# Kernel tuning notes

Hardware: AMD Instinct MI355X
Metric: run time of the kernel (lower is better)

Reference implementation:

```python
import math
import jax, jax.numpy as jnp
import numpy as np

B, N, NC = 2, 2048, 256
C_S, C_COND, C_Z, C_H, H, PQK, PV = 384, 256, 128, 16, 12, 4, 8
BQ, BK = 32, 128
NBLK = N // BQ
INF, EPS = 1e5, 1e-8
CONCAT = C_Z // 4 + C_H + PV * 4  # per-head output feature dim


def _ln(x, w=None, b=None, eps=1e-5):
    mu = jnp.mean(x, -1, keepdims=True)
    var = jnp.mean((x - mu) ** 2, -1, keepdims=True)
    y = (x - mu) * jax.lax.rsqrt(var + eps)
    if w is not None:
        y = y * w
    if b is not None:
        y = y + b
    return y


def _quat_to_rot(q):
    w, x, y, z = q[..., 0], q[..., 1], q[..., 2], q[..., 3]
    r = jnp.stack([
        1 - 2 * (y * y + z * z), 2 * (x * y - w * z), 2 * (x * z + w * y),
        2 * (x * y + w * z), 1 - 2 * (x * x + z * z), 2 * (y * z - w * x),
        2 * (x * z - w * y), 2 * (y * z + w * x), 1 - 2 * (x * x + y * y),
    ], axis=-1)
    return r.reshape(q.shape[:-1] + (3, 3))


def setup_inputs() -> dict:
    key = jax.random.key(0)
    ks = jax.random.split(key, 24)
    p = lambda k, shp: 0.02 * jax.random.normal(k, shp, dtype=jnp.float32)
    quat = jax.random.normal(ks[5], (B, N, 4), dtype=jnp.float32)
    quat = quat / jnp.linalg.norm(quat, axis=-1, keepdims=True)
    hc = H * C_H
    return {
        "s": jax.random.normal(ks[0], (B, N, C_S), dtype=jnp.float32),
        "cond": jax.random.normal(ks[1], (B, NC, C_COND), dtype=jnp.float32),
        "z": jax.random.normal(ks[2], (B, NBLK, BQ, BK, C_Z), dtype=jnp.float32),
        "trans": jax.random.normal(ks[3], (B, N, 3), dtype=jnp.float32),
        "rots": _quat_to_rot(quat),
        "s_mask": jnp.ones((B, N), dtype=jnp.float32),
        "cond_to_s_idx": jax.random.randint(ks[4], (B, N), 0, NC),
        "ln_cond_w": jnp.ones((C_COND,), dtype=jnp.float32),
        "lin_cond_W": p(ks[6], (C_S, C_COND)),
        "lin_cond_b": jnp.zeros((C_S,), dtype=jnp.float32),
        "lin_cond_nb_W": p(ks[7], (C_S, C_COND)),
        "ln_z_w": jnp.ones((C_Z,), dtype=jnp.float32),
        "ln_z_b": jnp.zeros((C_Z,), dtype=jnp.float32),
        "Wq": p(ks[8], (hc, C_S)),
        "Wk": p(ks[9], (hc, C_S)),
        "Wv": p(ks[10], (hc, C_S)),
        "Wqp": p(ks[11], (H * PQK * 3, C_S)),
        "Wkvp": p(ks[12], (H * (PQK + PV) * 3, C_S)),
        "Wb": p(ks[13], (H, C_Z)),
        "Wdz": p(ks[14], (C_Z // 4, C_Z)),
        "head_weights": jnp.full((H,), 0.541324854612918, dtype=jnp.float32),
        "Wout": p(ks[15], (C_S, H * CONCAT)),
    }


def _forward(s, cond, z, trans, rots, s_mask, cond_to_s_idx,
             ln_cond_w, lin_cond_W, lin_cond_b, lin_cond_nb_W, ln_z_w, ln_z_b,
             Wq, Wk, Wv, Wqp, Wkvp, Wb, Wdz, head_weights, Wout):
    # ---- GatherAdaLN ----
    s_n = _ln(s)
    c_n = _ln(cond, ln_cond_w)
    idx3 = jnp.broadcast_to(cond_to_s_idx[..., None], (B, N, C_S))
    gate = jnp.take_along_axis(c_n @ lin_cond_W.T + lin_cond_b, idx3, axis=1) * s_mask[..., None]
    bias = jnp.take_along_axis(c_n @ lin_cond_nb_W.T, idx3, axis=1) * s_mask[..., None]
    s2 = s_n * jax.nn.sigmoid(gate) + bias
    # ---- pair LN ----
    zn = _ln(z, ln_z_w, ln_z_b)
    # ---- block gather (to_queries / to_keys) ----
    pad = (BK - BQ) // 2
    base = jnp.arange(NBLK)[:, None] * BQ + jnp.arange(BK)[None, :] - pad  # [NBLK, BK]
    validk = (base >= 0) & (base < N)
    kidx = jnp.clip(base, 0, N - 1)

    def to_q(x):
        return x.reshape((B, NBLK, BQ) + x.shape[2:])

    def to_k(x):
        g = x[:, kidx]  # [B, NBLK, BK, ...]
        vm = validk.reshape((1, NBLK, BK) + (1,) * (g.ndim - 3)).astype(g.dtype)
        return g * vm

    q_in, k_in = to_q(s2), to_k(s2)
    q_t, q_R = to_q(trans), to_q(rots)
    k_t = to_k(trans)
    k_R = jnp.where(validk[None, :, :, None, None], rots[:, kidx], jnp.eye(3, dtype=rots.dtype))
    # ---- scalar q/k/v ----
    q = (q_in @ Wq.T).reshape(B, NBLK, BQ, H, C_H)
    k = (k_in @ Wk.T).reshape(B, NBLK, BK, H, C_H)
    v = (k_in @ Wv.T).reshape(B, NBLK, BK, H, C_H)
    # ---- point q/k/v in global frames ----
    qp = (q_in @ Wqp.T).reshape(B, NBLK, BQ, H * PQK, 3)
    q_pts = (jnp.einsum('bnqij,bnqpj->bnqpi', q_R, qp) + q_t[..., None, :]).reshape(B, NBLK, BQ, H, PQK, 3)
    kvp = (k_in @ Wkvp.T).reshape(B, NBLK, BK, H * (PQK + PV), 3)
    kv_pts = (jnp.einsum('bnkij,bnkpj->bnkpi', k_R, kvp) + k_t[..., None, :]).reshape(B, NBLK, BK, H, PQK + PV, 3)
    k_pts, v_pts = kv_pts[..., :PQK, :], kv_pts[..., PQK:, :]
    # ---- logits ----
    b_bias = zn @ Wb.T  # [B,NBLK,BQ,BK,H]
    a = jnp.einsum('bnqhc,bnkhc->bnqkh', q, k) * math.sqrt(1.0 / (3 * C_H)) + b_bias * math.sqrt(1.0 / 3)
    # point bias (cdist form)
    pt = -2.0 * jnp.einsum('bnqhpd,bnkhpd->bnqkh', q_pts, k_pts)
    pt = pt + jnp.sum(q_pts ** 2, axis=(-1, -2))[..., None, :]
    pt = pt + jnp.sum(k_pts ** 2, axis=(-1, -2))[..., None, :, :]
    hw = jax.nn.softplus(head_weights) * math.sqrt(1.0 / (3 * (PQK * 9.0 / 2)))
    pt = pt * hw * (-0.5)
    qm = to_q(s_mask[..., None])  # [B,NBLK,BQ,1]
    km = to_k(s_mask[..., None])  # [B,NBLK,BK,1]
    amask = INF * (qm * jnp.swapaxes(km, -1, -2) - 1.0)  # [B,NBLK,BQ,BK]
    a = a + pt + amask[..., None]
    a = jax.nn.softmax(jnp.swapaxes(a, -1, -2), axis=-1)  # [B,NBLK,BQ,H,BK]
    # ---- outputs ----
    o = jnp.einsum('bnqhk,bnkhc->bnqhc', a, v).reshape(B, NBLK, BQ, H * C_H)
    o_pt = jnp.einsum('bnqhk,bnkhvc->bnqhvc', a, v_pts)
    o_pt = jnp.einsum('bnqij,bnqhvi->bnqhvj', q_R, o_pt - q_t[..., None, None, :])  # R^T (p - t)
    o_pt_norm = jnp.sqrt(jnp.sum(o_pt ** 2, -1) + EPS).reshape(B, NBLK, BQ, H * PV)
    o_pt_flat = o_pt.reshape(B, NBLK, BQ, H * PV * 3)
    pair_z = zn @ Wdz.T  # [B,NBLK,BQ,BK,C_Z//4]
    o_pair = jnp.einsum('bnqhk,bnqkc->bnqhc', a, pair_z).reshape(B, NBLK, BQ, H * (C_Z // 4))
    feats = jnp.concatenate([o, o_pt_flat, o_pt_norm, o_pair], axis=-1)
    return (feats @ Wout.T).reshape(B, N, C_S)


def reference(s, cond, z, trans, rots, s_mask, cond_to_s_idx,
              ln_cond_w, lin_cond_W, lin_cond_b, lin_cond_nb_W, ln_z_w, ln_z_b,
              Wq, Wk, Wv, Wqp, Wkvp, Wb, Wdz, head_weights, Wout):
    return _forward(s, cond, z, trans, rots, s_mask, cond_to_s_idx,
                    ln_cond_w, lin_cond_W, lin_cond_b, lin_cond_nb_W, ln_z_w, ln_z_b,
                    Wq, Wk, Wv, Wqp, Wkvp, Wb, Wdz, head_weights, Wout)
```

## Files before the change

### kernel.cpp

```cpp
#include <hip/hip_runtime.h>
#include <math.h>

constexpr int Bv = 2, Nv = 2048, NCv = 256;
constexpr int CSv = 384, CCONDv = 256;
constexpr int CHv = 16, Hv = 12, PQKv = 4, PVv = 8;
constexpr int BQv = 32, BKv = 128, NBLKv = 64;
constexpr int HC = Hv * CHv;
constexpr int QPD = Hv * PQKv * 3;
constexpr int FEAT = 960;
constexpr int PROJW = 1152;
constexpr int NPAD = 2144;
constexpr float S1 = 0.14433756729740643f;
constexpr float S2 = 0.5773502691896258f;
constexpr float HWS = 0.13608276348795434f;

typedef __attribute__((ext_vector_type(8))) short bf16x8;
typedef __attribute__((ext_vector_type(4))) float f32x4;

__device__ __forceinline__ short f2bf(float f) {
    unsigned u = __float_as_uint(f);
    u += 0x7FFF + ((u >> 16) & 1);
    return (short)(u >> 16);
}
__device__ __forceinline__ float bf2f(short s) {
    return __uint_as_float(((unsigned)(unsigned short)s) << 16);
}
__device__ __forceinline__ unsigned pk2(short lo, short hi) {
    return ((unsigned)(unsigned short)lo) | (((unsigned)(unsigned short)hi) << 16);
}

union BF8 { short s[8]; bf16x8 v; uint4 u; };

__device__ __forceinline__ float blockReduceSum(float v, volatile float* red, int t, int nthr) {
    #pragma unroll
    for (int off = 32; off > 0; off >>= 1) v += __shfl_down(v, off, 64);
    int wid = t >> 6, lane = t & 63, nw = nthr >> 6;
    __syncthreads();
    if (lane == 0) red[wid] = v;
    __syncthreads();
    float r = 0.f;
    for (int w = 0; w < nw; ++w) r += red[w];
    return r;
}

__global__ __launch_bounds__(256) void k_head(const float* __restrict__ Wq,
                                              const float* __restrict__ Wk,
                                              const float* __restrict__ Wv,
                                              const float* __restrict__ Wqp,
                                              const float* __restrict__ Wkvp,
                                              const float* __restrict__ Wg,
                                              const float* __restrict__ Wnb,
                                              short* __restrict__ wsW,
                                              short* __restrict__ wsW2,
                                              const float* __restrict__ Wb,
                                              const float* __restrict__ Wdz,
                                              const float* __restrict__ lnzw,
                                              const float* __restrict__ lnzb,
                                              short* __restrict__ wp,
                                              float* __restrict__ SB,
                                              const float* __restrict__ cond,
                                              const float* __restrict__ lncw,
                                              short* __restrict__ cnbf) {
    __shared__ float red[4];
    int bid = blockIdx.x;
    int t = threadIdx.x;
    if (bid < 624) {
        int off = (bid * 256 + t) * 4;
        const float* src;
        int rel;
        if (off < 442368) {
            rel = off;
            if (rel < 73728) src = Wq;
            else if (rel < 147456) { src = Wk; rel -= 73728; }
            else if (rel < 221184) { src = Wv; rel -= 147456; }
            else if (rel < 276480) { src = Wqp; rel -= 221184; }
            else { src = Wkvp; rel -= 276480; }
            float4 v = *(const float4*)(src + rel);
            *(uint2*)(wsW + off) = make_uint2(pk2(f2bf(v.x), f2bf(v.y)), pk2(f2bf(v.z), f2bf(v.w)));
        } else {
            int o2 = off - 442368;
            rel = o2;
            if (rel < 98304) src = Wg; else { src = Wnb; rel -= 98304; }
            float4 v = *(const float4*)(src + rel);
            *(uint2*)(wsW2 + o2) = make_uint2(pk2(f2bf(v.x), f2bf(v.y)), pk2(f2bf(v.z), f2bf(v.w)));
        }
    } else if (bid == 624) {
        if (t < 176) {
            int c = t >> 2, q = t & 3;
            const float* wrow = (c < 12) ? (Wb + (size_t)c * 128) : (Wdz + (size_t)(c - 12) * 128);
            float sacc = 0.f, bacc = 0.f;
            for (int i = q * 32; i < q * 32 + 32; ++i) {
                float wf = wrow[i] * lnzw[i];
                short bs = f2bf(wf);
                wp[c * 128 + i] = bs;
                sacc += bf2f(bs);
                bacc += lnzb[i] * wrow[i];
            }
            sacc += __shfl_xor(sacc, 1, 64); sacc += __shfl_xor(sacc, 2, 64);
            bacc += __shfl_xor(bacc, 1, 64); bacc += __shfl_xor(bacc, 2, 64);
            if (q == 0) { SB[c] = sacc; SB[48 + c] = bacc; }
        }
        for (int i = t; i < 512; i += 256) wp[44 * 128 + i] = 0;
        if (t >= 176 && t < 180) { SB[t - 132] = 0.f; SB[48 + t - 132] = 0.f; }
    } else {
        int row = bid - 625;
        float c = cond[row * CCONDv + t];
        float mu = blockReduceSum(c, red, t, 256) * (1.f / CCONDv);
        float d = c - mu;
        float var = blockReduceSum(d * d, red, t, 256) * (1.f / CCONDv);
        cnbf[row * CCONDv + t] = f2bf(d * rsqrtf(var + 1e-5f) * lncw[t]);
    }
}

__global__ __launch_bounds__(256) void k_gemm_bt(const short* __restrict__ A,
                                                 const short* __restrict__ B,
                                                 float* __restrict__ C,
                                                 int K, int ldc) {
    __shared__ short As[128 * 40];
    __shared__ short Bs[128 * 40];
    int t = threadIdx.x;
    int m0 = blockIdx.x * 128, n0 = blockIdx.y * 128;
    int wv = t >> 6, lane = t & 63, lr = lane & 15, quad = lane >> 4;
    int mq = (wv & 1) * 64, nq = (wv >> 1) * 64;
    f32x4 acc[4][4];
    #pragma unroll
    for (int i = 0; i < 4; ++i)
        #pragma unroll
        for (int j = 0; j < 4; ++j) acc[i][j] = 0;

    int r0 = t >> 2, c8 = (t & 3) * 8;
    int r1 = (t + 256) >> 2, c81 = ((t + 256) & 3) * 8;

    for (int k0 = 0; k0 < K; k0 += 32) {
        uint4 a0 = *(const uint4*)(A + (size_t)(m0 + r0) * K + k0 + c8);
        uint4 a1 = *(const uint4*)(A + (size_t)(m0 + r1) * K + k0 + c81);
        uint4 b0 = *(const uint4*)(B + (size_t)(n0 + r0) * K + k0 + c8);
        uint4 b1 = *(const uint4*)(B + (size_t)(n0 + r1) * K + k0 + c81);
        *(uint4*)&As[r0 * 40 + c8] = a0;
        *(uint4*)&As[r1 * 40 + c81] = a1;
        *(uint4*)&Bs[r0 * 40 + c8] = b0;
        *(uint4*)&Bs[r1 * 40 + c81] = b1;
        __syncthreads();
        bf16x8 af[4], bf[4];
        #pragma unroll
        for (int i = 0; i < 4; ++i) {
            af[i] = *(const bf16x8*)&As[(mq + i * 16 + lr) * 40 + quad * 8];
            bf[i] = *(const bf16x8*)&Bs[(nq + i * 16 + lr) * 40 + quad * 8];
        }
        #pragma unroll
        for (int i = 0; i < 4; ++i)
            #pragma unroll
            for (int j = 0; j < 4; ++j)
                acc[i][j] = __builtin_amdgcn_mfma_f32_16x16x32_bf16(af[i], bf[j], acc[i][j], 0, 0, 0);
        __syncthreads();
    }
    #pragma unroll
    for (int i = 0; i < 4; ++i) {
        #pragma unroll
        for (int j = 0; j < 4; ++j) {
            int col = n0 + nq + j * 16 + lr;
            #pragma unroll
            for (int r = 0; r < 4; ++r) {
                int row = m0 + mq + i * 16 + quad * 4 + r;
                C[(size_t)row * ldc + col] = acc[i][j][r];
            }
        }
    }
}

__global__ __launch_bounds__(128) void k_s2(const float* __restrict__ s,
                                            const float* __restrict__ gb,
                                            const float* __restrict__ bg,
                                            const int* __restrict__ cidx,
                                            const float* __restrict__ smask,
                                            short* __restrict__ s2bf) {
    __shared__ float red[4];
    int row = blockIdx.x;
    int t = threadIdx.x;
    const float* sr = s + (size_t)row * CSv;
    float x0 = sr[t], x1 = sr[t + 128], x2 = sr[t + 256];
    float mu = blockReduceSum(x0 + x1 + x2, red, t, 128) * (1.f / CSv);
    float d0 = x0 - mu, d1 = x1 - mu, d2 = x2 - mu;
    float var = blockReduceSum(d0 * d0 + d1 * d1 + d2 * d2, red, t, 128) * (1.f / CSv);
    float rs = rsqrtf(var + 1e-5f);
    int b = row / Nv;
    int ci = cidx[row];
    float m = smask[row];
    const float* gbr = gb + (size_t)(b * NCv + ci) * 768;
    float dd[3] = {d0, d1, d2};
    #pragma unroll
    for (int j = 0; j < 3; ++j) {
        int cc = t + j * 128;
        float sn = dd[j] * rs;
        float g = (gbr[cc] + bg[cc]) * m, bi = gbr[384 + cc] * m;
        s2bf[(size_t)row * CSv + cc] = f2bf(sn * (1.f / (1.f + expf(-g))) + bi);
    }
}

__global__ __launch_bounds__(192) void k_post(const float* __restrict__ proj,
                                              const float* __restrict__ rots,
                                              const float* __restrict__ trans,
                                              float* __restrict__ qpts,
                                              float* __restrict__ kpts,
                                              float* __restrict__ vpts,
                                              float* __restrict__ qsq,
                                              float* __restrict__ ksq) {
    __shared__ float R[9], tr[3];
    int row = blockIdx.x;
    int t = threadIdx.x;
    if (t < 9) R[t] = rots[(size_t)row * 9 + t];
    if (t < 3) tr[t] = trans[(size_t)row * 3 + t];
    __syncthreads();
    const float* pr = proj + (size_t)row * PROJW + 576;
    float x = pr[t * 3 + 0], y = pr[t * 3 + 1], z = pr[t * 3 + 2];
    float ox = R[0] * x + R[1] * y + R[2] * z + tr[0];
    float oy = R[3] * x + R[4] * y + R[5] * z + tr[1];
    float oz = R[6] * x + R[7] * y + R[8] * z + tr[2];
    float sq = ox * ox + oy * oy + oz * oz;
    if (t < 48) {
        qpts[(size_t)row * QPD + t * 3 + 0] = ox;
        qpts[(size_t)row * QPD + t * 3 + 1] = oy;
        qpts[(size_t)row * QPD + t * 3 + 2] = oz;
        float s4 = sq + __shfl_xor(sq, 1, 64);
        s4 += __shfl_xor(s4, 2, 64);
        if ((t & 3) == 0) qsq[(size_t)row * Hv + (t >> 2)] = s4;
    } else {
        int p = t - 48;
        int h = p / 12, pp = p % 12;
        if (pp < PQKv) {
            kpts[(size_t)row * QPD + (h * PQKv + pp) * 3 + 0] = ox;
            kpts[(size_t)row * QPD + (h * PQKv + pp) * 3 + 1] = oy;
            kpts[(size_t)row * QPD + (h * PQKv + pp) * 3 + 2] = oz;
            float s4 = sq + __shfl_xor(sq, 1, 64);
            s4 += __shfl_xor(s4, 2, 64);
            if (pp == 0) ksq[(size_t)row * Hv + h] = s4;
        } else {
            int vi = h * PVv + pp - PQKv;
            vpts[(size_t)row * (Hv * PVv * 3) + vi * 3 + 0] = ox;
            vpts[(size_t)row * (Hv * PVv * 3) + vi * 3 + 1] = oy;
            vpts[(size_t)row * (Hv * PVv * 3) + vi * 3 + 2] = oz;
        }
    }
}

__global__ __launch_bounds__(256) void k_zg(const float* __restrict__ z,
                                            const short* __restrict__ wp,
                                            const float* __restrict__ SB,
                                            short* __restrict__ bbias2,
                                            short* __restrict__ pairzT,
                                            const short* __restrict__ cnbf,
                                            const short* __restrict__ wsW2,
                                            float* __restrict__ gb) {
    extern __shared__ char smem[];
    int t = threadIdx.x;
    int bid = blockIdx.x;
    if (bid >= 4096) {
        short* As = (short*)smem;
        short* Bs = As + 128 * 40;
        int g = bid - 4096;
        int m0 = (g & 3) * 128, n0 = (g >> 2) * 128;
        const int K = CCONDv, ldc = 768;
        int wv = t >> 6, lane = t & 63, lr = lane & 15, quad = lane >> 4;
        int mq = (wv & 1) * 64, nq = (wv >> 1) * 64;
        f32x4 acc[4][4];
        #pragma unroll
        for (int i = 0; i < 4; ++i)
            #pragma unroll
            for (int j = 0; j < 4; ++j) acc[i][j] = 0;
        int r0 = t >> 2, c8 = (t & 3) * 8;
        int r1 = (t + 256) >> 2, c81 = ((t + 256) & 3) * 8;
        for (int k0 = 0; k0 < K; k0 += 32) {
            uint4 a0 = *(const uint4*)(cnbf + (size_t)(m0 + r0) * K + k0 + c8);
            uint4 a1 = *(const uint4*)(cnbf + (size_t)(m0 + r1) * K + k0 + c81);
            uint4 b0 = *(const uint4*)(wsW2 + (size_t)(n0 + r0) * K + k0 + c8);
            uint4 b1 = *(const uint4*)(wsW2 + (size_t)(n0 + r1) * K + k0 + c81);
            *(uint4*)&As[r0 * 40 + c8] = a0;
            *(uint4*)&As[r1 * 40 + c81] = a1;
            *(uint4*)&Bs[r0 * 40 + c8] = b0;
            *(uint4*)&Bs[r1 * 40 + c81] = b1;
            __syncthreads();
            bf16x8 af[4], bf[4];
            #pragma unroll
            for (int i = 0; i < 4; ++i) {
                af[i] = *(const bf16x8*)&As[(mq + i * 16 + lr) * 40 + quad * 8];
                bf[i] = *(const bf16x8*)&Bs[(nq + i * 16 + lr) * 40 + quad * 8];
            }
            #pragma unroll
            for (int i = 0; i < 4; ++i)
                #pragma unroll
                for (int j = 0; j < 4; ++j)
                    acc[i][j] = __builtin_amdgcn_mfma_f32_16x16x32_bf16(af[i], bf[j], acc[i][j], 0, 0, 0);
            __syncthreads();
        }
        #pragma unroll
        for (int i = 0; i < 4; ++i)
            #pragma unroll
            for (int j = 0; j < 4; ++j) {
                int col = n0 + nq + j * 16 + lr;
                #pragma unroll
                for (int r = 0; r < 4; ++r) {
                    int row = m0 + mq + i * 16 + quad * 4 + r;
                    gb[(size_t)row * ldc + col] = acc[i][j][r];
                }
            }
        return;
    }
    short* zbuf = (short*)smem;
    short* wbuf = zbuf + 128 * 136;
    float* muL  = (float*)(wbuf + 48 * 136);
    float* rsL  = muL + 128;
    float* SL   = rsL + 128;
    float* BL   = SL + 48;

    int bblk = bid >> 5, qq = bid & 31;
    size_t row0 = (size_t)bid * 128;

    for (int idx = t; idx < 768; idx += 256) {
        int c = idx >> 4, k8 = idx & 15;
        uint4 v = *(const uint4*)(wp + c * 128 + k8 * 8);
        *(uint4*)&wbuf[c * 136 + k8 * 8] = v;
    }
    if (t < 96) {
        float v = SB[t];
        if (t < 48) SL[t] = v; else BL[t - 48] = v;
    }

    const float4* zsrc = (const float4*)(z + row0 * 128);
    #pragma unroll
    for (int it = 0; it < 16; ++it) {
        int f = it * 256 + t;
        int r = f >> 5, c4 = f & 31;
        float4 v = zsrc[f];
        short s0 = f2bf(v.x), s1 = f2bf(v.y), s2v = f2bf(v.z), s3 = f2bf(v.w);
        *(uint2*)&zbuf[r * 136 + c4 * 4] = make_uint2(pk2(s0, s1), pk2(s2v, s3));
        float sm = v.x + v.y + v.z + v.w;
        float sq = v.x * v.x + v.y * v.y + v.z * v.z + v.w * v.w;
        #pragma unroll
        for (int off = 1; off <= 16; off <<= 1) {
            sm += __shfl_xor(sm, off, 64);
            sq += __shfl_xor(sq, off, 64);
        }
        if ((t & 31) == 0) {
            float mu = sm * (1.f / 128.f);
            float var = sq * (1.f / 128.f) - mu * mu;
            muL[r] = mu;
            rsL[r] = rsqrtf(var + 1e-5f);
        }
    }
    __syncthreads();

    int wv = t >> 6, lane = t & 63;
    int lr = lane & 15, quad = lane >> 4;
    int mb = wv * 32;
    f32x4 acc[2][3];
    #pragma unroll
    for (int i = 0; i < 2; ++i)
        #pragma unroll
        for (int j = 0; j < 3; ++j) acc[i][j] = 0;
    #pragma unroll
    for (int kt = 0; kt < 4; ++kt) {
        int ko = kt * 32 + quad * 8;
        bf16x8 a0 = *(const bf16x8*)&zbuf[(mb + lr) * 136 + ko];
        bf16x8 a1 = *(const bf16x8*)&zbuf[(mb + 16 + lr) * 136 + ko];
        bf16x8 b0 = *(const bf16x8*)&wbuf[lr * 136 + ko];
        bf16x8 b1 = *(const bf16x8*)&wbuf[(16 + lr) * 136 + ko];
        bf16x8 b2 = *(const bf16x8*)&wbuf[(32 + lr) * 136 + ko];
        acc[0][0] = __builtin_amdgcn_mfma_f32_16x16x32_bf16(a0, b0, acc[0][0], 0, 0, 0);
        acc[0][1] = __builtin_amdgcn_mfma_f32_16x16x32_bf16(a0, b1, acc[0][1], 0, 0, 0);
        acc[0][2] = __builtin_amdgcn_mfma_f32_16x16x32_bf16(a0, b2, acc[0][2], 0, 0, 0);
        acc[1][0] = __builtin_amdgcn_mfma_f32_16x16x32_bf16(a1, b0, acc[1][0], 0, 0, 0);
        acc[1][1] = __builtin_amdgcn_mfma_f32_16x16x32_bf16(a1, b1, acc[1][1], 0, 0, 0);
        acc[1][2] = __builtin_amdgcn_mfma_f32_16x16x32_bf16(a1, b2, acc[1][2], 0, 0, 0);
    }

    short* bb_base = bbias2 + (size_t)(bblk * 12) * 4096 + qq * 128;
    short* pz_base = pairzT + (size_t)bid * 32 * 128;
    #pragma unroll
    for (int mt = 0; mt < 2; ++mt) {
        #pragma unroll
        for (int nt = 0; nt < 3; ++nt) {
            int col = nt * 16 + lr;
            int kbase = mb + mt * 16 + quad * 4;
            float ov[4];
            #pragma unroll
            for (int r4 = 0; r4 < 4; ++r4) {
                int rl = kbase + r4;
                ov[r4] = rsL[rl] * (acc[mt][nt][r4] - muL[rl] * SL[col]) + BL[col];
            }
            if (col < 12) {
                *(uint2*)&bb_base[(size_t)col * 4096 + kbase] =
                    make_uint2(pk2(f2bf(S2 * ov[0]), f2bf(S2 * ov[1])),
                               pk2(f2bf(S2 * ov[2]), f2bf(S2 * ov[3])));
            } else if (col < 44) {
                int c = col - 12;
                *(uint2*)&pz_base[c * 128 + kbase] =
                    make_uint2(pk2(f2bf(ov[0]), f2bf(ov[1])), pk2(f2bf(ov[2]), f2bf(ov[3])));
            }
        }
    }
}

__global__ __launch_bounds__(256) void k_kvcache(const float* __restrict__ proj,
                                                 const float* __restrict__ qpts,
                                                 const float* __restrict__ kpts,
                                                 const float* __restrict__ vpts,
                                                 const float* __restrict__ qsq,
                                                 const float* __restrict__ ksq,
                                                 const float* __restrict__ smask,
                                                 const float* __restrict__ head_w,
                                                 short* __restrict__ kc,
                                                 short* __restrict__ qc,
                                                 short* __restrict__ vTc,
                                                 float* __restrict__ cb,
                                                 float* __restrict__ rb,
                                                 float* __restrict__ kmp) {
    __shared__ short vt[40 * 136];
    int t = threadIdx.x;
    int tile = blockIdx.x % 17;
    int bh = blockIdx.x / 17;
    int b = bh / 12, h = bh % 12;
    float hw = log1pf(expf(head_w[h])) * HWS;
    int pn0 = tile * 128;
    int npn = (pn0 + 128 <= NPAD) ? 128 : (NPAD - pn0);

    for (int i = t; i < npn * 4; i += 256) {
        int r = i >> 2, q = i & 3;
        int pn = pn0 + r;
        int n = pn - 48; n = n < 0 ? 0 : (n > Nv - 1 ? Nv - 1 : n);
        size_t g = (size_t)b * Nv + n;
        BF8 o;
        if (q < 2) {
            const float* src = proj + g * PROJW + 192 + h * 16 + q * 8;
            #pragma unroll
            for (int j = 0; j < 8; ++j) o.s[j] = f2bf(src[j]);
        } else if (q == 2) {
            const float* src = kpts + g * QPD + h * 12;
            #pragma unroll
            for (int j = 0; j < 8; ++j) o.s[j] = f2bf(src[j]);
        } else {
            const float* src = kpts + g * QPD + h * 12 + 8;
            #pragma unroll
            for (int j = 0; j < 4; ++j) o.s[j] = f2bf(src[j]);
            o.s[4] = o.s[5] = o.s[6] = o.s[7] = 0;
        }
        *(uint4*)&kc[(((size_t)bh) * NPAD + pn) * 32 + q * 8] = o.u;
    }
    for (int i = t; i < npn; i += 256) {
        int pn = pn0 + i;
        int n = pn - 48; n = n < 0 ? 0 : (n > Nv - 1 ? Nv - 1 : n);
        size_t g = (size_t)b * Nv + n;
        cb[(size_t)bh * NPAD + pn] = -0.5f * hw * ksq[g * Hv + h];
        if (h == 0) kmp[(size_t)b * NPAD + pn] = (pn >= 48 && pn < 48 + Nv) ? smask[g] : 0.f;
    }
    for (int i = t; i < 512; i += 256) {
        int r = i >> 2, q = i & 3;
        int n = pn0 - 48 + r;
        if (n >= 0 && n < Nv) {
            size_t g = (size_t)b * Nv + n;
            BF8 o;
            if (q < 2) {
                const float* src = proj + g * PROJW + h * 16 + q * 8;
                #pragma unroll
                for (int j = 0; j < 8; ++j) o.s[j] = f2bf(S1 * src[j]);
            } else if (q == 2) {
                const float* src = qpts + g * QPD + h * 12;
                #pragma unroll
                for (int j = 0; j < 8; ++j) o.s[j] = f2bf(hw * src[j]);
            } else {
                const float* src = qpts + g * QPD + h * 12 + 8;
                #pragma unroll
                for (int j = 0; j < 4; ++j) o.s[j] = f2bf(hw * src[j]);
                o.s[4] = o.s[5] = o.s[6] = o.s[7] = 0;
            }
            *(uint4*)&qc[(((size_t)bh) * Nv + n) * 32 + q * 8] = o.u;
            if (q == 0) rb[(size_t)bh * Nv + n] = -0.5f * hw * qsq[g * Hv + h];
        }
    }
    for (int i = t; i < npn * 10; i += 256) {
        int r = i / 10, q = i % 10;
        int pn = pn0 + r;
        int n = pn - 48; n = n < 0 ? 0 : (n > Nv - 1 ? Nv - 1 : n);
        size_t g = (size_t)b * Nv + n;
        float4 v = (q < 4) ? *(const float4*)&proj[g * PROJW + 384 + h * 16 + q * 4]
                           : *(const float4*)&vpts[g * (Hv * PVv * 3) + h * 24 + (q - 4) * 4];
        int c0 = q * 4;
        vt[(c0 + 0) * 136 + r] = f2bf(v.x);
        vt[(c0 + 1) * 136 + r] = f2bf(v.y);
        vt[(c0 + 2) * 136 + r] = f2bf(v.z);
        vt[(c0 + 3) * 136 + r] = f2bf(v.w);
    }
    __syncthreads();
    for (int i = t; i < 640; i += 256) {
        int c = i >> 4, s = i & 15;
        if (s * 8 < npn)
            *(uint4*)&vTc[((size_t)bh * 40 + c) * NPAD + pn0 + s * 8] = *(const uint4*)&vt[c * 136 + s * 8];
    }
}

__global__ __launch_bounds__(512, 6) void k_attn_main(const short* __restrict__ kc,
                                                      const short* __restrict__ qc,
                                                      const short* __restrict__ vTc,
                                                      const float* __restrict__ cb,
                                                      const float* __restrict__ rb,
                                                      const float* __restrict__ kmp,
                                                      const float* __restrict__ smask,
                                                      const short* __restrict__ bbias2,
                                                      short* __restrict__ Aws,
                                                      float* __restrict__ optraw,
                                                      float* __restrict__ feats) {
    __shared__ short kfrag[128 * 40];
    __shared__ short qfrag[32 * 40];
    __shared__ short vtileT[48 * 136];
    __shared__ float sc[32 * 132];
    __shared__ short Abuf[32 * 136];
    __shared__ float rowb[32], qmL[32], colb[128], kmL[128];

    int t = threadIdx.x;
    int hp = blockIdx.x % 6;
    int bblk = blockIdx.x / 6;
    int b = bblk >> 6, blk = bblk & 63;
    int wv = t >> 6, lane = t & 63;
    int lr = lane & 15, quad = lane >> 4;
    int n0 = blk * BQv;

    if (t < 128) kmL[t] = kmp[(size_t)b * NPAD + n0 + t];
    if (t < 32)  qmL[t] = smask[(size_t)b * Nv + n0 + t];
    {
        int c = 40 + (t >> 6), k2 = (t & 63) * 2;
        *(unsigned*)&vtileT[c * 136 + k2] = 0;
    }
    __syncthreads();

    for (int hh = 0; hh < 2; ++hh) {
        int h = hp * 2 + hh;
        size_t bh = (size_t)b * 12 + h;

        {
            int r = t >> 2, s8 = (t & 3) * 8;
            *(uint4*)&kfrag[r * 40 + s8] = *(const uint4*)&kc[(bh * NPAD + n0 + r) * 32 + s8];
        }
        if (t < 128) {
            int r = t >> 2, s8 = (t & 3) * 8;
            *(uint4*)&qfrag[r * 40 + s8] = *(const uint4*)&qc[(bh * Nv + n0 + r) * 32 + s8];
        }
        if (t < 128) colb[t] = cb[bh * NPAD + n0 + t];
        if (t < 32)  rowb[t] = rb[bh * Nv + n0 + t];
        for (int i = t; i < 640; i += 512) {
            int c = i >> 4, s8 = (i & 15) * 8;
            *(uint4*)&vtileT[c * 136 + s8] = *(const uint4*)&vTc[(bh * 40 + c) * NPAD + n0 + s8];
        }
        __syncthreads();

        f32x4 d[2];
        d[0] = 0; d[1] = 0;
        {
            bf16x8 bfr = *(const bf16x8*)&kfrag[(wv * 16 + lr) * 40 + quad * 8];
            bf16x8 a0 = *(const bf16x8*)&qfrag[lr * 40 + quad * 8];
            bf16x8 a1 = *(const bf16x8*)&qfrag[(16 + lr) * 40 + quad * 8];
            d[0] = __builtin_amdgcn_mfma_f32_16x16x32_bf16(a0, bfr, d[0], 0, 0, 0);
            d[1] = __builtin_amdgcn_mfma_f32_16x16x32_bf16(a1, bfr, d[1], 0, 0, 0);
        }
        {
            const short* bb = bbias2 + (size_t)(bblk * 12 + h) * 4096;
            #pragma unroll
            for (int mt = 0; mt < 2; ++mt) {
                #pragma unroll
                for (int r = 0; r < 4; ++r) {
                    int q = mt * 16 + quad * 4 + r;
                    int k = wv * 16 + lr;
                    float logit = d[mt][r] + rowb[q] + colb[k]
                                + 1e5f * (qmL[q] * kmL[k] - 1.f)
                                + bf2f(bb[q * 128 + k]);
                    sc[q * 132 + k] = logit;
                }
            }
        }
        __syncthreads();

        {
            int q = t >> 4, i0 = (t & 15) * 8;
            float v[8];
            float m = -3.0e38f;
            #pragma unroll
            for (int j = 0; j < 8; ++j) { v[j] = sc[q * 132 + i0 + j]; m = fmaxf(m, v[j]); }
            #pragma unroll
            for (int off = 1; off <= 8; off <<= 1) m = fmaxf(m, __shfl_xor(m, off, 64));
            float ssum = 0.f;
            #pragma unroll
            for (int j = 0; j < 8; ++j) { v[j] = __expf(v[j] - m); ssum += v[j]; }
            #pragma unroll
            for (int off = 1; off <= 8; off <<= 1) ssum += __shfl_xor(ssum, off, 64);
            float inv = 1.f / ssum;
            short a8[8];
            #pragma unroll
            for (int j = 0; j < 8; ++j) a8[j] = f2bf(v[j] * inv);
            uint4 packed = make_uint4(pk2(a8[0], a8[1]), pk2(a8[2], a8[3]),
                                      pk2(a8[4], a8[5]), pk2(a8[6], a8[7]));
            *(uint4*)&Abuf[q * 136 + i0] = packed;
            *(uint4*)&Aws[((size_t)(bblk * 32 + q) * 12 + h) * 128 + i0] = packed;
        }
        __syncthreads();

        if (wv < 6) {
            int mt = wv & 1, nt = wv >> 1;
            f32x4 acc = 0;
            #pragma unroll
            for (int kt = 0; kt < 4; ++kt) {
                bf16x8 a = *(const bf16x8*)&Abuf[(mt * 16 + lr) * 136 + quad * 8 + kt * 32];
                bf16x8 bv = *(const bf16x8*)&vtileT[(nt * 16 + lr) * 136 + quad * 8 + kt * 32];
                acc = __builtin_amdgcn_mfma_f32_16x16x32_bf16(a, bv, acc, 0, 0, 0);
            }
            int c = nt * 16 + lr;
            #pragma unroll
            for (int r = 0; r < 4; ++r) {
                int q = mt * 16 + quad * 4 + r;
                size_t nqg = (size_t)b * Nv + n0 + q;
                if (c < 16) feats[nqg * FEAT + h * 16 + c] = acc[r];
                else if (c < 40) optraw[nqg * 288 + h * 24 + (c - 16)] = acc[r];
            }
        }
        __syncthreads();
    }
}

__global__ __launch_bounds__(64) void k_pair(const short* __restrict__ Aws,
                                             const short* __restrict__ pairzT,
                                             const float* __restrict__ optraw,
                                             const float* __restrict__ rots,
                                             const float* __restrict__ trans,
                                             float* __restrict__ feats) {
    __shared__ float Rt[12];
    int t = threadIdx.x;
    int bid = blockIdx.x;
    int lr = t & 15, quad = t >> 4;

    if (t < 9) Rt[t] = rots[(size_t)bid * 9 + t];
    if (t < 3) Rt[9 + t] = trans[(size_t)bid * 3 + t];
    __syncthreads();

    const short* Ab = Aws + (size_t)bid * 1536;
    const short* Pb = pairzT + (size_t)bid * 4096;
    f32x4 acc0 = 0, acc1 = 0;
    #pragma unroll
    for (int kt = 0; kt < 4; ++kt) {
        int ko = kt * 32 + quad * 8;
        bf16x8 a = 0;
        if (lr < 12) a = *(const bf16x8*)&Ab[lr * 128 + ko];
        bf16x8 b0 = *(const bf16x8*)&Pb[lr * 128 + ko];
        bf16x8 b1 = *(const bf16x8*)&Pb[(16 + lr) * 128 + ko];
        acc0 = __builtin_amdgcn_mfma_f32_16x16x32_bf16(a, b0, acc0, 0, 0, 0);
        acc1 = __builtin_amdgcn_mfma_f32_16x16x32_bf16(a, b1, acc1, 0, 0, 0);
    }
    float* frow = feats + (size_t)bid * FEAT;
    #pragma unroll
    for (int r = 0; r < 4; ++r) {
        int hh = quad * 4 + r;
        if (hh < 12) {
            frow[576 + hh * 32 + lr] = acc0[r];
            frow[576 + hh * 32 + 16 + lr] = acc1[r];
        }
    }

    for (int p = t; p < 96; p += 64) {
        float x = optraw[(size_t)bid * 288 + p * 3 + 0] - Rt[9];
        float y = optraw[(size_t)bid * 288 + p * 3 + 1] - Rt[10];
        float z = optraw[(size_t)bid * 288 + p * 3 + 2] - Rt[11];
        float lx = Rt[0] * x + Rt[3] * y + Rt[6] * z;
        float ly = Rt[1] * x + Rt[4] * y + Rt[7] * z;
        float lz = Rt[2] * x + Rt[5] * y + Rt[8] * z;
        frow[192 + p * 3 + 0] = lx;
        frow[192 + p * 3 + 1] = ly;
        frow[192 + p * 3 + 2] = lz;
        frow[480 + p] = sqrtf(lx * lx + ly * ly + lz * lz + 1e-8f);
    }
}

__global__ __launch_bounds__(256) void k_out(const float* __restrict__ A,
                                             const float* __restrict__ Wo,
                                             float* __restrict__ C) {
    __shared__ float As[32][68];
    __shared__ float Bs[32][68];
    int t = threadIdx.x;
    int m0 = blockIdx.x * 64;
    int c0 = blockIdx.y * 64;
    int tx = t & 15, ty = t >> 4;
    int lr = t >> 2, lk = (t & 3) * 8;
    float acc[4][4] = {};
    for (int k0 = 0; k0 < FEAT; k0 += 32) {
        const float4* ap = (const float4*)(A + (size_t)(m0 + lr) * FEAT + k0 + lk);
        const float4* bp = (const float4*)(Wo + (size_t)(c0 + lr) * FEAT + k0 + lk);
        float4 a0 = ap[0], a1 = ap[1];
        float4 b0 = bp[0], b1 = bp[1];
        As[lk + 0][lr] = a0.x; As[lk + 1][lr] = a0.y; As[lk + 2][lr] = a0.z; As[lk + 3][lr] = a0.w;
        As[lk + 4][lr] = a1.x; As[lk + 5][lr] = a1.y; As[lk + 6][lr] = a1.z; As[lk + 7][lr] = a1.w;
        Bs[lk + 0][lr] = b0.x; Bs[lk + 1][lr] = b0.y; Bs[lk + 2][lr] = b0.z; Bs[lk + 3][lr] = b0.w;
        Bs[lk + 4][lr] = b1.x; Bs[lk + 5][lr] = b1.y; Bs[lk + 6][lr] = b1.z; Bs[lk + 7][lr] = b1.w;
        __syncthreads();
        #pragma unroll
        for (int kk = 0; kk < 32; ++kk) {
            float4 a4 = *(const float4*)&As[kk][ty * 4];
            float4 b4 = *(const float4*)&Bs[kk][tx * 4];
            float av[4] = {a4.x, a4.y, a4.z, a4.w};
            float bv[4] = {b4.x, b4.y, b4.z, b4.w};
            #pragma unroll
            for (int i = 0; i < 4; ++i)
                #pragma unroll
                for (int j = 0; j < 4; ++j) acc[i][j] += av[i] * bv[j];
        }
        __syncthreads();
    }
    #pragma unroll
    for (int i = 0; i < 4; ++i)
        #pragma unroll
        for (int j = 0; j < 4; ++j)
            C[(size_t)(m0 + ty * 4 + i) * CSv + c0 + tx * 4 + j] = acc[i][j];
}

extern "C" void kernel_launch(void* const* d_in, const int* in_sizes, int n_in,
                              void* d_out, int out_size, void* d_ws, size_t ws_size,
                              hipStream_t stream) {
    const float* s          = (const float*)d_in[0];
    const float* cond       = (const float*)d_in[1];
    const float* z          = (const float*)d_in[2];
    const float* trans      = (const float*)d_in[3];
    const float* rots       = (const float*)d_in[4];
    const float* smask      = (const float*)d_in[5];
    const int*   cidx       = (const int*)d_in[6];
    const float* ln_cond_w  = (const float*)d_in[7];
    const float* lin_cond_W = (const float*)d_in[8];
    const float* lin_cond_b = (const float*)d_in[9];
    const float* lin_cond_nb_W = (const float*)d_in[10];
    const float* ln_z_w     = (const float*)d_in[11];
    const float* ln_z_b     = (const float*)d_in[12];
    const float* Wq         = (const float*)d_in[13];
    const float* Wk         = (const float*)d_in[14];
    const float* Wv         = (const float*)d_in[15];
    const float* Wqp        = (const float*)d_in[16];
    const float* Wkvp       = (const float*)d_in[17];
    const float* Wb         = (const float*)d_in[18];
    const float* Wdz        = (const float*)d_in[19];
    const float* head_w     = (const float*)d_in[20];
    const float* Wout       = (const float*)d_in[21];
    float* out = (float*)d_out;

    float* p = (float*)d_ws;
    short* wp = (short*)p; p += 3072;
    float* SBp = p; p += 96;
    short* wsW  = (short*)p; p += 221184;
    short* wsW2 = (short*)p; p += 98304;
    short* cnbf = (short*)p; p += 65536;
    float* gb   = p; p += (size_t)512 * 768;
    short* s2bf = (short*)p; p += (size_t)Bv * Nv * CSv / 2;
    float* proj = p; p += (size_t)Bv * Nv * PROJW;
    float* qpts = p; p += (size_t)Bv * Nv * QPD;
    float* kpts = p; p += (size_t)Bv * Nv * QPD;
    float* vpts = p; p += (size_t)Bv * Nv * (Hv * PVv * 3);
    float* qsq  = p; p += (size_t)Bv * Nv * Hv;
    float* ksq  = p; p += (size_t)Bv * Nv * Hv;
    short* bbias2 = (short*)p; p += (size_t)128 * 12 * 4096 / 2;
    short* pairzT = (short*)p; p += (size_t)128 * 32 * 32 * 64;
    short* Aws    = (short*)p; p += (size_t)4096 * 12 * 64;
    float* optraw = p; p += (size_t)4096 * 288;
    float* feats  = p; p += (size_t)Bv * Nv * FEAT;
    short* kc  = (short*)p; p += (size_t)Bv * 12 * NPAD * 32 / 2;
    short* qc  = (short*)p; p += (size_t)Bv * 12 * Nv * 32 / 2;
    short* vTc = (short*)p; p += (size_t)Bv * 12 * 40 * NPAD / 2;
    float* cbw = p; p += (size_t)Bv * 12 * NPAD;
    float* rbw = p; p += (size_t)Bv * 12 * Nv;
    float* kmp = p; p += (size_t)Bv * NPAD;

    k_head<<<1137, 256, 0, stream>>>(Wq, Wk, Wv, Wqp, Wkvp, lin_cond_W, lin_cond_nb_W,
                                     wsW, wsW2, Wb, Wdz, ln_z_w, ln_z_b, wp, SBp,
                                     cond, ln_cond_w, cnbf);
    k_zg<<<4120, 256, 49280, stream>>>(z, wp, SBp, bbias2, pairzT, cnbf, wsW2, gb);
    k_s2<<<Bv * Nv, 128, 0, stream>>>(s, gb, lin_cond_b, cidx, smask, s2bf);
    k_gemm_bt<<<dim3(32, 9), 256, 0, stream>>>(s2bf, wsW, proj, CSv, PROJW);
    k_post<<<Bv * Nv, 192, 0, stream>>>(proj, rots, trans, qpts, kpts, vpts, qsq, ksq);
    k_kvcache<<<Bv * 12 * 17, 256, 0, stream>>>(proj, qpts, kpts, vpts, qsq, ksq,
                                                smask, head_w, kc, qc, vTc, cbw, rbw, kmp);
    k_attn_main<<<Bv * NBLKv * 6, 512, 0, stream>>>(kc, qc, vTc, cbw, rbw, kmp, smask,
                                                    bbias2, Aws, optraw, feats);
    k_pair<<<Bv * NBLKv * BQv, 64, 0, stream>>>(Aws, pairzT, optraw, rots, trans, feats);
    k_out<<<dim3(64, 6), 256, 0, stream>>>(feats, Wout, out);
}
```

Baseline: 580.3 us.

## Move output projection to split-bf16 MFMA and halve projection GEMM N-tile

Replaces the FP32 SIMT output GEMM with an MFMA kernel that splits both operands into bf16 hi/lo parts and sums three products, keeping close to FP32 accuracy. Wout is pre-split once in the head kernel, using extra blocks. The projection GEMM switches to 128x64 tiles, doubling the block count to fill more CUs. The cost is three times the MFMA work, extra workspace, and per-tile conversion of the activations.

```diff
diff --git a/kernel.cpp b/kernel.cpp
--- a/kernel.cpp
+++ b/kernel.cpp
@@ -27,6 +27,10 @@
 }
 __device__ __forceinline__ unsigned pk2(short lo, short hi) {
     return ((unsigned)(unsigned short)lo) | (((unsigned)(unsigned short)hi) << 16);
+}
+__device__ __forceinline__ void split2(float x, short& hi, short& lo) {
+    hi = f2bf(x);
+    lo = f2bf(x - bf2f(hi));
 }
 
 union BF8 { short s[8]; bf16x8 v; uint4 u; };
@@ -60,7 +64,10 @@
                                               float* __restrict__ SB,
                                               const float* __restrict__ cond,
                                               const float* __restrict__ lncw,
-                                              short* __restrict__ cnbf) {
+                                              short* __restrict__ cnbf,
+                                              const float* __restrict__ Wout,
+                                              short* __restrict__ WoutH,
+                                              short* __restrict__ WoutL) {
     __shared__ float red[4];
     int bid = blockIdx.x;
     int t = threadIdx.x;
@@ -102,62 +109,65 @@
         }
         for (int i = t; i < 512; i += 256) wp[44 * 128 + i] = 0;
         if (t >= 176 && t < 180) { SB[t - 132] = 0.f; SB[48 + t - 132] = 0.f; }
-    } else {
+    } else if (bid < 1137) {
         int row = bid - 625;
         float c = cond[row * CCONDv + t];
         float mu = blockReduceSum(c, red, t, 256) * (1.f / CCONDv);
         float d = c - mu;
         float var = blockReduceSum(d * d, red, t, 256) * (1.f / CCONDv);
         cnbf[row * CCONDv + t] = f2bf(d * rsqrtf(var + 1e-5f) * lncw[t]);
-    }
-}
-
-__global__ __launch_bounds__(256) void k_gemm_bt(const short* __restrict__ A,
-                                                 const short* __restrict__ B,
-                                                 float* __restrict__ C,
-                                                 int K, int ldc) {
+    } else {
+        int off = ((bid - 1137) * 256 + t) * 4;
+        float4 v = *(const float4*)(Wout + off);
+        short h0, l0, h1, l1, h2, l2, h3, l3;
+        split2(v.x, h0, l0); split2(v.y, h1, l1); split2(v.z, h2, l2); split2(v.w, h3, l3);
+        *(uint2*)(WoutH + off) = make_uint2(pk2(h0, h1), pk2(h2, h3));
+        *(uint2*)(WoutL + off) = make_uint2(pk2(l0, l1), pk2(l2, l3));
+    }
+}
+
+__global__ __launch_bounds__(256) void k_gemm_proj(const short* __restrict__ A,
+                                                   const short* __restrict__ B,
+                                                   float* __restrict__ C) {
     __shared__ short As[128 * 40];
-    __shared__ short Bs[128 * 40];
+    __shared__ short Bs[64 * 40];
+    const int K = CSv, ldc = PROJW;
     int t = threadIdx.x;
-    int m0 = blockIdx.x * 128, n0 = blockIdx.y * 128;
+    int m0 = blockIdx.x * 128, n0 = blockIdx.y * 64;
     int wv = t >> 6, lane = t & 63, lr = lane & 15, quad = lane >> 4;
-    int mq = (wv & 1) * 64, nq = (wv >> 1) * 64;
-    f32x4 acc[4][4];
+    int mq = (wv & 1) * 64, nq = (wv >> 1) * 32;
+    f32x4 acc[4][2];
     #pragma unroll
     for (int i = 0; i < 4; ++i)
         #pragma unroll
-        for (int j = 0; j < 4; ++j) acc[i][j] = 0;
+        for (int j = 0; j < 2; ++j) acc[i][j] = 0;
 
     int r0 = t >> 2, c8 = (t & 3) * 8;
-    int r1 = (t + 256) >> 2, c81 = ((t + 256) & 3) * 8;
 
     for (int k0 = 0; k0 < K; k0 += 32) {
         uint4 a0 = *(const uint4*)(A + (size_t)(m0 + r0) * K + k0 + c8);
-        uint4 a1 = *(const uint4*)(A + (size_t)(m0 + r1) * K + k0 + c81);
+        uint4 a1 = *(const uint4*)(A + (size_t)(m0 + r0 + 64) * K + k0 + c8);
         uint4 b0 = *(const uint4*)(B + (size_t)(n0 + r0) * K + k0 + c8);
-        uint4 b1 = *(const uint4*)(B + (size_t)(n0 + r1) * K + k0 + c81);
         *(uint4*)&As[r0 * 40 + c8] = a0;
-        *(uint4*)&As[r1 * 40 + c81] = a1;
+        *(uint4*)&As[(r0 + 64) * 40 + c8] = a1;
         *(uint4*)&Bs[r0 * 40 + c8] = b0;
-        *(uint4*)&Bs[r1 * 40 + c81] = b1;
         __syncthreads();
-        bf16x8 af[4], bf[4];
-        #pragma unroll
-        for (int i = 0; i < 4; ++i) {
-            af[i] = *(const bf16x8*)&As[(mq + i * 16 + lr) * 40 + quad * 8];
-            bf[i] = *(const bf16x8*)&Bs[(nq + i * 16 + lr) * 40 + quad * 8];
-        }
+        bf16x8 af[4], bf[2];
+        #pragma unroll
+        for (int i = 0; i < 4; ++i) af[i] = *(const bf16x8*)&As[(mq + i * 16 + lr) * 40 + quad * 8];
+        #pragma unroll
+        for (int j = 0; j < 2; ++j) bf[j] = *(const bf16x8*)&Bs[(nq + j * 16 + lr) * 40 + quad * 8];
         #pragma unroll
         for (int i = 0; i < 4; ++i)
             #pragma unroll
-            for (int j = 0; j < 4; ++j)
+            for (int j = 0; j < 2; ++j)
                 acc[i][j] = __builtin_amdgcn_mfma_f32_16x16x32_bf16(af[i], bf[j], acc[i][j], 0, 0, 0);
         __syncthreads();
     }
     #pragma unroll
     for (int i = 0; i < 4; ++i) {
         #pragma unroll
-        for (int j = 0; j < 4; ++j) {
+        for (int j = 0; j < 2; ++j) {
             int col = n0 + nq + j * 16 + lr;
             #pragma unroll
             for (int r = 0; r < 4; ++r) {
@@ -675,45 +685,72 @@
     }
 }
 
-__global__ __launch_bounds__(256) void k_out(const float* __restrict__ A,
-                                             const float* __restrict__ Wo,
-                                             float* __restrict__ C) {
-    __shared__ float As[32][68];
-    __shared__ float Bs[32][68];
+__global__ __launch_bounds__(256) void k_out_mfma(const float* __restrict__ A,
+                                                  const short* __restrict__ BhG,
+                                                  const short* __restrict__ BlG,
+                                                  float* __restrict__ C) {
+    __shared__ short Ah[32 * 40];
+    __shared__ short Al[32 * 40];
+    __shared__ short Bh[128 * 40];
+    __shared__ short Bl[128 * 40];
     int t = threadIdx.x;
-    int m0 = blockIdx.x * 64;
-    int c0 = blockIdx.y * 64;
-    int tx = t & 15, ty = t >> 4;
-    int lr = t >> 2, lk = (t & 3) * 8;
-    float acc[4][4] = {};
+    int m0 = blockIdx.x * 32, c0 = blockIdx.y * 128;
+    int wv = t >> 6, lane = t & 63, lr = lane & 15, quad = lane >> 4;
+    int nq = wv * 32;
+    f32x4 acc[2][2];
+    acc[0][0] = 0; acc[0][1] = 0; acc[1][0] = 0; acc[1][1] = 0;
+
+    int ra = t >> 3, ca = (t & 7) * 4;
+    int rb = t >> 2, s8 = (t & 3) * 8;
+
     for (int k0 = 0; k0 < FEAT; k0 += 32) {
-        const float4* ap = (const float4*)(A + (size_t)(m0 + lr) * FEAT + k0 + lk);
-        const float4* bp = (const float4*)(Wo + (size_t)(c0 + lr) * FEAT + k0 + lk);
-        float4 a0 = ap[0], a1 = ap[1];
-        float4 b0 = bp[0], b1 = bp[1];
-        As[lk + 0][lr] = a0.x; As[lk + 1][lr] = a0.y; As[lk + 2][lr] = a0.z; As[lk + 3][lr] = a0.w;
-        As[lk + 4][lr] = a1.x; As[lk + 5][lr] = a1.y; As[lk + 6][lr] = a1.z; As[lk + 7][lr] = a1.w;
-        Bs[lk + 0][lr] = b0.x; Bs[lk + 1][lr] = b0.y; Bs[lk + 2][lr] = b0.z; Bs[lk + 3][lr] = b0.w;
-        Bs[lk + 4][lr] = b1.x; Bs[lk + 5][lr] = b1.y; Bs[lk + 6][lr] = b1.z; Bs[lk + 7][lr] = b1.w;
+        float4 av = *(const float4*)(A + (size_t)(m0 + ra) * FEAT + k0 + ca);
+        short h0, l0, h1, l1, h2, l2, h3, l3;
+        split2(av.x, h0, l0); split2(av.y, h1, l1); split2(av.z, h2, l2); split2(av.w, h3, l3);
+        uint4 bh0 = *(const uint4*)(BhG + (size_t)(c0 + rb) * FEAT + k0 + s8);
+        uint4 bh1 = *(const uint4*)(BhG + (size_t)(c0 + rb + 64) * FEAT + k0 + s8);
+        uint4 bl0 = *(const uint4*)(BlG + (size_t)(c0 + rb) * FEAT + k0 + s8);
+        uint4 bl1 = *(const uint4*)(BlG + (size_t)(c0 + rb + 64) * FEAT + k0 + s8);
+        *(uint2*)&Ah[ra * 40 + ca] = make_uint2(pk2(h0, h1), pk2(h2, h3));
+        *(uint2*)&Al[ra * 40 + ca] = make_uint2(pk2(l0, l1), pk2(l2, l3));
+        *(uint4*)&Bh[rb * 40 + s8] = bh0;
+        *(uint4*)&Bh[(rb + 64) * 40 + s8] = bh1;
+        *(uint4*)&Bl[rb * 40 + s8] = bl0;
+        *(uint4*)&Bl[(rb + 64) * 40 + s8] = bl1;
         __syncthreads();
-        #pragma unroll
-        for (int kk = 0; kk < 32; ++kk) {
-            float4 a4 = *(const float4*)&As[kk][ty * 4];
-            float4 b4 = *(const float4*)&Bs[kk][tx * 4];
-            float av[4] = {a4.x, a4.y, a4.z, a4.w};
-            float bv[4] = {b4.x, b4.y, b4.z, b4.w};
-            #pragma unroll
-            for (int i = 0; i < 4; ++i)
-                #pragma unroll
-                for (int j = 0; j < 4; ++j) acc[i][j] += av[i] * bv[j];
-        }
+        bf16x8 ah[2], al[2], bh[2], bl[2];
+        #pragma unroll
+        for (int mi = 0; mi < 2; ++mi) {
+            ah[mi] = *(const bf16x8*)&Ah[(mi * 16 + lr) * 40 + quad * 8];
+            al[mi] = *(const bf16x8*)&Al[(mi * 16 + lr) * 40 + quad * 8];
+        }
+        #pragma unroll
+        for (int nj = 0; nj < 2; ++nj) {
+            bh[nj] = *(const bf16x8*)&Bh[(nq + nj * 16 + lr) * 40 + quad * 8];
+            bl[nj] = *(const bf16x8*)&Bl[(nq + nj * 16 + lr) * 40 + quad * 8];
+        }
+        #pragma unroll
+        for (int mi = 0; mi < 2; ++mi)
+            #pragma unroll
+            for (int nj = 0; nj < 2; ++nj) {
+                acc[mi][nj] = __builtin_amdgcn_mfma_f32_16x16x32_bf16(ah[mi], bh[nj], acc[mi][nj], 0, 0, 0);
+                acc[mi][nj] = __builtin_amdgcn_mfma_f32_16x16x32_bf16(ah[mi], bl[nj], acc[mi][nj], 0, 0, 0);
+                acc[mi][nj] = __builtin_amdgcn_mfma_f32_16x16x32_bf16(al[mi], bh[nj], acc[mi][nj], 0, 0, 0);
+            }
         __syncthreads();
     }
     #pragma unroll
-    for (int i = 0; i < 4; ++i)
-        #pragma unroll
-        for (int j = 0; j < 4; ++j)
-            C[(size_t)(m0 + ty * 4 + i) * CSv + c0 + tx * 4 + j] = acc[i][j];
+    for (int mi = 0; mi < 2; ++mi) {
+        #pragma unroll
+        for (int nj = 0; nj < 2; ++nj) {
+            int col = c0 + nq + nj * 16 + lr;
+            #pragma unroll
+            for (int r = 0; r < 4; ++r) {
+                int row = m0 + mi * 16 + quad * 4 + r;
+                C[(size_t)row * CSv + col] = acc[mi][nj][r];
+            }
+        }
+    }
 }
 
 extern "C" void kernel_launch(void* const* d_in, const int* in_sizes, int n_in,
@@ -768,18 +805,20 @@
     float* cbw = p; p += (size_t)Bv * 12 * NPAD;
     float* rbw = p; p += (size_t)Bv * 12 * Nv;
     float* kmp = p; p += (size_t)Bv * NPAD;
-
-    k_head<<<1137, 256, 0, stream>>>(Wq, Wk, Wv, Wqp, Wkvp, lin_cond_W, lin_cond_nb_W,
+    short* WoutH = (short*)p; p += (size_t)CSv * FEAT / 2;
+    short* WoutL = (short*)p; p += (size_t)CSv * FEAT / 2;
+
+    k_head<<<1497, 256, 0, stream>>>(Wq, Wk, Wv, Wqp, Wkvp, lin_cond_W, lin_cond_nb_W,
                                      wsW, wsW2, Wb, Wdz, ln_z_w, ln_z_b, wp, SBp,
-                                     cond, ln_cond_w, cnbf);
+                                     cond, ln_cond_w, cnbf, Wout, WoutH, WoutL);
     k_zg<<<4120, 256, 49280, stream>>>(z, wp, SBp, bbias2, pairzT, cnbf, wsW2, gb);
     k_s2<<<Bv * Nv, 128, 0, stream>>>(s, gb, lin_cond_b, cidx, smask, s2bf);
-    k_gemm_bt<<<dim3(32, 9), 256, 0, stream>>>(s2bf, wsW, proj, CSv, PROJW);
+    k_gemm_proj<<<dim3(32, 18), 256, 0, stream>>>(s2bf, wsW, proj);
     k_post<<<Bv * Nv, 192, 0, stream>>>(proj, rots, trans, qpts, kpts, vpts, qsq, ksq);
     k_kvcache<<<Bv * 12 * 17, 256, 0, stream>>>(proj, qpts, kpts, vpts, qsq, ksq,
                                                 smask, head_w, kc, qc, vTc, cbw, rbw, kmp);
     k_attn_main<<<Bv * NBLKv * 6, 512, 0, stream>>>(kc, qc, vTc, cbw, rbw, kmp, smask,
                                                     bbias2, Aws, optraw, feats);
     k_pair<<<Bv * NBLKv * BQv, 64, 0, stream>>>(Aws, pairzT, optraw, rots, trans, feats);
-    k_out<<<dim3(64, 6), 256, 0, stream>>>(feats, Wout, out);
-}
+    k_out_mfma<<<dim3(128, 3), 256, 0, stream>>>(feats, WoutH, WoutL, out);
+}
```

Result: faster. 548.2 us (-5.5%).
